# Optimization experiments

Hardware: AMD Instinct MI355X
Metric: run time of the kernel (lower is better)

Reference implementation:

```python
import jax, jax.numpy as jnp
import numpy as np

B, N, M, H, NH = 8, 1024, 512, 1024, 4
DH = H // NH          # 256 main attention head size
CDH = (H // 4) // 4   # 64  cross attention qk head size
EPS = 1e-12


def _ln(x, g, b):
    mu = jnp.mean(x, axis=-1, keepdims=True)
    var = jnp.mean((x - mu) ** 2, axis=-1, keepdims=True)
    return (x - mu) / jnp.sqrt(var + EPS) * g + b


def _heads(x, nh):
    b, n, d = x.shape
    return x.reshape(b, n, nh, d // nh).transpose(0, 2, 1, 3)  # [b,nh,n,dh]


def setup_inputs() -> dict:
    key = jax.random.key(0)
    ks = iter(jax.random.split(key, 64))
    nk = lambda: next(ks)
    w = lambda *s: jax.random.normal(nk(), s, jnp.float32) * 0.02
    inp = {}
    inp["hidden_states"] = jax.random.normal(nk(), (B, N, H), jnp.float32)
    inp["attention_mask"] = jnp.ones((B, N), jnp.float32)
    inp["structure_mask"] = (jax.random.uniform(nk(), (B, 3, N, N)) < 0.2).astype(jnp.float32)
    inp["Sentence_em"] = w(1, B, N, H)
    inp["entity_id_em"] = w(1, B, N, H)
    inp["cross_struct_mask"] = (jax.random.uniform(nk(), (B, 1, N, M)) < 0.3).astype(jnp.float32)
    inp["encoder_hidden_states"] = jax.random.normal(nk(), (1, B, M, H), jnp.float32)
    inp["encoder_attention_mask"] = jnp.ones((B, M), jnp.float32)
    # ---- Struct_SelfAttention params ----
    inp["Wq"] = w(H, 3 * DH); inp["bq"] = jnp.zeros(3 * DH)
    inp["Wk"] = w(H, 3 * DH); inp["bk"] = jnp.zeros(3 * DH)
    inp["Wv"] = w(H, H);      inp["bv"] = jnp.zeros(H)
    inp["Wq1"] = w(H, DH);    inp["bq1"] = jnp.zeros(DH)
    inp["Wk1"] = w(H, DH);    inp["bk1"] = jnp.zeros(DH)
    inp["ln_g"] = jnp.ones(H); inp["ln_b"] = jnp.zeros(H)
    inp["gnn_W"] = w(H, H); inp["gnn_b"] = jnp.zeros(H)
    inp["gnn_ln_g"] = jnp.ones(H); inp["gnn_ln_b"] = jnp.zeros(H)
    # ---- Cross_Attention params ----
    inp["cWq"] = w(H, H // 4); inp["cbq"] = jnp.zeros(H // 4)
    inp["cWk"] = w(H, H // 4); inp["cbk"] = jnp.zeros(H // 4)
    inp["cWv"] = w(H, H);      inp["cbv"] = jnp.zeros(H)
    inp["cWo"] = w(H, H);      inp["cbo"] = jnp.zeros(H)
    inp["cWg"] = w(2 * H, H);  inp["cbg"] = jnp.full((H,), -1.0, jnp.float32)  # Gate bias init -1
    inp["c_ln_g"] = jnp.ones(H); inp["c_ln_b"] = jnp.zeros(H)
    # ---- Output block params ----
    inp["oW1"] = w(H, H); inp["ob1"] = jnp.zeros(H)
    inp["o_ln1_g"] = jnp.ones(H); inp["o_ln1_b"] = jnp.zeros(H)
    inp["oW2"] = w(H, 2 * H); inp["ob2"] = jnp.zeros(2 * H)
    inp["oW3"] = w(2 * H, H); inp["ob3"] = jnp.zeros(H)
    inp["o_ln3_g"] = jnp.ones(H); inp["o_ln3_b"] = jnp.zeros(H)
    inp["layer_idx"] = 0
    return inp


def reference(hidden_states, attention_mask, structure_mask, Sentence_em, entity_id_em,
              cross_struct_mask, encoder_hidden_states, encoder_attention_mask,
              Wq, bq, Wk, bk, Wv, bv, Wq1, bq1, Wk1, bk1, ln_g, ln_b,
              gnn_W, gnn_b, gnn_ln_g, gnn_ln_b,
              cWq, cbq, cWk, cbk, cWv, cbv, cWo, cbo, cWg, cbg, c_ln_g, c_ln_b,
              oW1, ob1, o_ln1_g, o_ln1_b, oW2, ob2, oW3, ob3, o_ln3_g, o_ln3_b,
              layer_idx):
    hs = hidden_states
    q = _heads(hs @ Wq + bq, 3)          # [B,3,N,DH]
    k = _heads(hs @ Wk + bk, 3)
    v = _heads(hs @ Wv + bv, 4)          # [B,4,N,DH]
    s1 = jnp.einsum('bhnd,bhmd->bhnm', q, k)          # unscaled scores, 3 heads
    am0 = (1.0 - attention_mask)[:, None, None, :] * -10000.0
    s3 = s1 + am0
    # valid off-diagonal pairs mask (broadcasts over the 3 heads)
    pair = attention_mask[:, None, :, None] * attention_mask[:, None, None, :]
    idxw = ((pair * (1.0 - jnp.eye(N, dtype=jnp.float32))) > 0.5).astype(jnp.float32)  # [B,1,N,N]
    # sigmoid focal loss (gamma=2, alpha=0.25, mean over selected elements)
    p = jax.nn.sigmoid(s3)
    t = structure_mask
    fl = 0.25 * t * (1.0 - p) ** 2 * (-jax.nn.log_sigmoid(s3)) \
       + 0.75 * (1.0 - t) * p ** 2 * (-jax.nn.log_sigmoid(-s3))
    loss = jnp.sum(fl * idxw) / (3.0 * jnp.sum(idxw))
    # structural attention path (3 heads)
    s1 = s1 / np.float32(np.sqrt(DH)) + (1.0 - structure_mask) * -10000.0
    probs1 = jax.nn.softmax(s1, axis=-1)
    # positional/structural single-head path
    h1 = _ln(hs + Sentence_em[layer_idx] + entity_id_em[layer_idx], ln_g, ln_b)
    q1 = _heads(h1 @ Wq1 + bq1, 1)
    k1 = _heads(h1 @ Wk1 + bk1, 1)
    s2 = jnp.einsum('bhnd,bhmd->bhnm', q1, k1) / np.float32(np.sqrt(DH)) + am0
    probs2 = jax.nn.softmax(s2, axis=-1)
    probs = jnp.concatenate([probs2, probs1], axis=1)  # [B,4,N,N]
    ctx = jnp.einsum('bhnm,bhmd->bhnd', probs, v).transpose(0, 2, 1, 3).reshape(B, N, H)
    gnn_out = _ln(ctx @ gnn_W + gnn_b, gnn_ln_g, gnn_ln_b)
    # ---- Cross attention ----
    enc = encoder_hidden_states[layer_idx]            # [B,M,H]
    cq = _heads(gnn_out @ cWq + cbq, 4)               # [B,4,N,CDH]
    ck = _heads(enc @ cWk + cbk, 4)                   # [B,4,M,CDH]
    cv = _heads(enc @ cWv + cbv, 4)                   # [B,4,M,DH]
    cs = jnp.einsum('bhnd,bhmd->bhnm', cq, ck) / np.float32(np.sqrt(CDH))
    cs = cs + (1.0 - cross_struct_mask) * -10000.0
    cp = jax.nn.softmax(cs, axis=-1)
    cctx = jnp.einsum('bhnm,bhmd->bhnd', cp, cv).transpose(0, 2, 1, 3).reshape(B, N, H)
    cctx = cctx @ cWo + cbo
    gate = jax.nn.sigmoid(jnp.concatenate([gnn_out, cctx], axis=-1) @ cWg + cbg)
    cross_out = _ln(gate * cctx + (1.0 - gate) * gnn_out, c_ln_g, c_ln_b)
    # ---- Output block (gated FFN) ----
    h = _ln(cross_out @ oW1 + ob1 + hidden_states, o_ln1_g, o_ln1_b)
    h3 = jax.nn.gelu(h @ oW2 + ob2, approximate=False) @ oW3 + ob3
    out = _ln(h3 + h, o_ln3_g, o_ln3_b)
    return out, loss
```

## Files before the change

### kernel.cpp

```cpp
#include <hip/hip_runtime.h>
#include <math.h>

#define DEV __device__ __forceinline__

typedef short short8 __attribute__((ext_vector_type(8)));
typedef float float4v __attribute__((ext_vector_type(4)));

DEV unsigned short f2bf(float f) {
    union { float f; unsigned u; } v; v.f = f;
    unsigned r = v.u + 0x7FFFu + ((v.u >> 16) & 1u);
    return (unsigned short)(r >> 16);
}

DEV float block_reduce(float v, int mode) {
    #pragma unroll
    for (int off = 32; off; off >>= 1) {
        float o = __shfl_xor(v, off);
        v = mode ? fmaxf(v, o) : (v + o);
    }
    __shared__ float sbuf[4];
    __syncthreads();
    if ((threadIdx.x & 63) == 0) sbuf[threadIdx.x >> 6] = v;
    __syncthreads();
    float r = sbuf[0];
    #pragma unroll
    for (int w = 1; w < 4; w++) r = mode ? fmaxf(r, sbuf[w]) : (r + sbuf[w]);
    return r;
}

template <bool BIAS, bool ACCUM, bool GELU>
__global__ __launch_bounds__(256) void gemm_bf16_kernel(
    const unsigned short* __restrict__ A, int lda,
    const unsigned short* __restrict__ Bt, int ldb,
    const float* __restrict__ bias,
    float* __restrict__ Cf, unsigned short* __restrict__ Cb,
    int N, int K)
{
    __shared__ unsigned short As[128 * 40];
    __shared__ unsigned short Bs[128 * 40];
    const int tid = threadIdx.x;
    const int w = tid >> 6, lane = tid & 63;
    const int l15 = lane & 15, quad = lane >> 4;
    const int m0 = blockIdx.y * 128, n0 = blockIdx.x * 128;
    const int wm = (w >> 1) * 64, wn = (w & 1) * 64;

    float4v acc[4][4];
    #pragma unroll
    for (int i = 0; i < 4; i++)
        #pragma unroll
        for (int j = 0; j < 4; j++) acc[i][j] = (float4v){0.f, 0.f, 0.f, 0.f};

    for (int k0 = 0; k0 < K; k0 += 32) {
        __syncthreads();
        #pragma unroll
        for (int i = 0; i < 2; i++) {
            const int c = tid + i * 256;
            const int row = c >> 2, kc = (c & 3) * 8;
            *(uint4*)(As + row * 40 + kc) =
                *(const uint4*)(A + (size_t)(m0 + row) * lda + k0 + kc);
            *(uint4*)(Bs + row * 40 + kc) =
                *(const uint4*)(Bt + (size_t)(n0 + row) * ldb + k0 + kc);
        }
        __syncthreads();
        short8 Af[4], Bf[4];
        #pragma unroll
        for (int mt = 0; mt < 4; mt++)
            Af[mt] = *(const short8*)(As + (wm + mt * 16 + l15) * 40 + quad * 8);
        #pragma unroll
        for (int nt = 0; nt < 4; nt++)
            Bf[nt] = *(const short8*)(Bs + (wn + nt * 16 + l15) * 40 + quad * 8);
        #pragma unroll
        for (int mt = 0; mt < 4; mt++)
            #pragma unroll
            for (int nt = 0; nt < 4; nt++)
                acc[mt][nt] = __builtin_amdgcn_mfma_f32_16x16x32_bf16(
                    Af[mt], Bf[nt], acc[mt][nt], 0, 0, 0);
    }

    #pragma unroll
    for (int nt = 0; nt < 4; nt++) {
        const int n = n0 + wn + nt * 16 + l15;
        const float bv = BIAS ? bias[n] : 0.f;
        #pragma unroll
        for (int mt = 0; mt < 4; mt++) {
            #pragma unroll
            for (int r = 0; r < 4; r++) {
                const int m = m0 + wm + mt * 16 + quad * 4 + r;
                const size_t off = (size_t)m * N + n;
                float v = acc[mt][nt][r] + bv;
                if (ACCUM) v += Cf[off];
                if (GELU) v = 0.5f * v * (1.f + erff(v * 0.70710678118654752f));
                if (Cf) Cf[off] = v;
                if (Cb) Cb[off] = f2bf(v);
            }
        }
    }
}

__global__ __launch_bounds__(256) void wtrans_kernel(
    const float* __restrict__ W, unsigned short* __restrict__ Wt, int K, int N)
{
    __shared__ float t[32][33];
    const int n0 = blockIdx.x * 32, k0 = blockIdx.y * 32;
    const int c = threadIdx.x & 31, r8 = threadIdx.x >> 5;
    #pragma unroll
    for (int i = 0; i < 4; i++) {
        const int r = r8 + i * 8;
        t[r][c] = W[(size_t)(k0 + r) * N + n0 + c];
    }
    __syncthreads();
    #pragma unroll
    for (int i = 0; i < 4; i++) {
        const int r = r8 + i * 8;
        Wt[(size_t)(n0 + r) * K + k0 + c] = f2bf(t[c][r]);
    }
}

__global__ __launch_bounds__(256) void trans_kernel(
    const unsigned short* __restrict__ v, unsigned short* __restrict__ Vt,
    int R, int C)
{
    __shared__ unsigned short t[32][33];
    const int b = blockIdx.z, r0 = blockIdx.x * 32, c0 = blockIdx.y * 32;
    const int c = threadIdx.x & 31, r8 = threadIdx.x >> 5;
    #pragma unroll
    for (int i = 0; i < 4; i++) {
        const int r = r8 + i * 8;
        t[r][c] = v[((size_t)b * R + r0 + r) * C + c0 + c];
    }
    __syncthreads();
    #pragma unroll
    for (int i = 0; i < 4; i++) {
        const int r = r8 + i * 8;
        Vt[((size_t)b * C + c0 + r) * R + r0 + c] = t[c][r];
    }
}

__global__ __launch_bounds__(256) void castbf_kernel(
    const float* __restrict__ x, unsigned short* __restrict__ y)
{
    const size_t i = ((size_t)blockIdx.x * 256 + threadIdx.x) * 4;
    float4 v = *(const float4*)(x + i);
    ushort4 o;
    o.x = f2bf(v.x); o.y = f2bf(v.y); o.z = f2bf(v.z); o.w = f2bf(v.w);
    *(ushort4*)(y + i) = o;
}

DEV void ln_finish(float4 xv, const float* __restrict__ g,
                   const float* __restrict__ bb, float* __restrict__ outf,
                   unsigned short* __restrict__ outb, size_t base)
{
    float s  = xv.x + xv.y + xv.z + xv.w;
    float s2 = xv.x * xv.x + xv.y * xv.y + xv.z * xv.z + xv.w * xv.w;
    #pragma unroll
    for (int off = 32; off; off >>= 1) {
        s += __shfl_xor(s, off);
        s2 += __shfl_xor(s2, off);
    }
    __shared__ float sa[4], sb[4];
    if ((threadIdx.x & 63) == 0) {
        sa[threadIdx.x >> 6] = s; sb[threadIdx.x >> 6] = s2;
    }
    __syncthreads();
    s  = sa[0] + sa[1] + sa[2] + sa[3];
    s2 = sb[0] + sb[1] + sb[2] + sb[3];
    const float mu  = s * (1.f / 1024.f);
    const float var = fmaxf(s2 * (1.f / 1024.f) - mu * mu, 0.f);
    const float inv = rsqrtf(var + 1e-12f);
    const int tid = threadIdx.x;
    float4 gv = ((const float4*)g)[tid];
    float4 bv = ((const float4*)bb)[tid];
    float4 o;
    o.x = (xv.x - mu) * inv * gv.x + bv.x;
    o.y = (xv.y - mu) * inv * gv.y + bv.y;
    o.z = (xv.z - mu) * inv * gv.z + bv.z;
    o.w = (xv.w - mu) * inv * gv.w + bv.w;
    if (outf) ((float4*)(outf + base))[tid] = o;
    if (outb) {
        ushort4 ob;
        ob.x = f2bf(o.x); ob.y = f2bf(o.y); ob.z = f2bf(o.z); ob.w = f2bf(o.w);
        ((ushort4*)(outb + base))[tid] = ob;
    }
}

__global__ __launch_bounds__(256) void ln_kernel(
    const float* __restrict__ x, const float* __restrict__ r1,
    const float* __restrict__ r2, const float* __restrict__ g,
    const float* __restrict__ bb, float* __restrict__ outf,
    unsigned short* __restrict__ outb)
{
    const size_t base = (size_t)blockIdx.x * 1024;
    const int tid = threadIdx.x;
    float4 xv = ((const float4*)(x + base))[tid];
    if (r1) {
        float4 a = ((const float4*)(r1 + base))[tid];
        xv.x += a.x; xv.y += a.y; xv.z += a.z; xv.w += a.w;
    }
    if (r2) {
        float4 a = ((const float4*)(r2 + base))[tid];
        xv.x += a.x; xv.y += a.y; xv.z += a.z; xv.w += a.w;
    }
    ln_finish(xv, g, bb, outf, outb, base);
}

__global__ __launch_bounds__(256) void gate_ln_kernel(
    const float* __restrict__ gpre, const float* __restrict__ co,
    const float* __restrict__ gn, const float* __restrict__ g,
    const float* __restrict__ bb, float* __restrict__ outf,
    unsigned short* __restrict__ outb)
{
    const size_t base = (size_t)blockIdx.x * 1024;
    const int tid = threadIdx.x;
    float4 gp = ((const float4*)(gpre + base))[tid];
    float4 cv = ((const float4*)(co + base))[tid];
    float4 gv = ((const float4*)(gn + base))[tid];
    float4 xv; float s;
    s = 1.f / (1.f + __expf(-gp.x)); xv.x = s * cv.x + (1.f - s) * gv.x;
    s = 1.f / (1.f + __expf(-gp.y)); xv.y = s * cv.y + (1.f - s) * gv.y;
    s = 1.f / (1.f + __expf(-gp.z)); xv.z = s * cv.z + (1.f - s) * gv.z;
    s = 1.f / (1.f + __expf(-gp.w)); xv.w = s * cv.w + (1.f - s) * gv.w;
    ln_finish(xv, g, bb, outf, outb, base);
}

__global__ __launch_bounds__(256) void attn_mfma_kernel(
    const unsigned short* __restrict__ qh,
    const unsigned short* __restrict__ kh,
    const unsigned short* __restrict__ q1,
    const unsigned short* __restrict__ k1,
    const unsigned short* __restrict__ Vt,
    const float* __restrict__ am,
    const float* __restrict__ smask,
    unsigned short* __restrict__ ctx,
    float* __restrict__ nump, float* __restrict__ denp)
{
    const int nb = blockIdx.x;
    const int h  = blockIdx.y;
    const int b  = blockIdx.z;
    const int tid = threadIdx.x;
    const int w = tid >> 6, lane = tid & 63;
    const int l15 = lane & 15, quad = lane >> 4;
    const int n0 = nb * 64;

    __shared__ unsigned short Ks[32 * 264];
    __shared__ unsigned short Vs[256 * 40];
    __shared__ unsigned short Ps[4][16 * 40];

    const unsigned short* qsrc; const unsigned short* ksrc; int kpitch, koff;
    if (h == 0) { qsrc = q1; ksrc = k1; kpitch = 256; koff = 0; }
    else        { qsrc = qh; ksrc = kh; kpitch = 768; koff = (h - 1) * 256; }

    short8 Qf[8];
    {
        const unsigned short* qrow =
            qsrc + (size_t)(b * 1024 + n0 + w * 16 + l15) * kpitch + koff;
        #pragma unroll
        for (int kk = 0; kk < 8; kk++)
            Qf[kk] = *(const short8*)(qrow + kk * 32 + quad * 8);
    }

    float4v O[16];
    #pragma unroll
    for (int i = 0; i < 16; i++) O[i] = (float4v){0.f, 0.f, 0.f, 0.f};
    float lsum[4] = {0.f, 0.f, 0.f, 0.f};
    float flsum = 0.f, dencnt = 0.f;
    const int nrow_base = n0 + w * 16 + quad * 4;
    float amn[4];
    #pragma unroll
    for (int r = 0; r < 4; r++) amn[r] = am[b * 1024 + nrow_base + r];
    const float* smbase = (h > 0)
        ? smask + ((size_t)b * 3 + (h - 1)) * 1024 * 1024 : nullptr;

    for (int m0 = 0; m0 < 1024; m0 += 32) {
        __syncthreads();
        for (int c = tid; c < 1024; c += 256) {
            const int row = c >> 5, kc = (c & 31) * 8;
            *(uint4*)(Ks + row * 264 + kc) =
                *(const uint4*)(ksrc + (size_t)(b * 1024 + m0 + row) * kpitch + koff + kc);
        }
        for (int c = tid; c < 1024; c += 256) {
            const int d = c >> 2, mc = (c & 3) * 8;
            *(uint4*)(Vs + d * 40 + mc) =
                *(const uint4*)(Vt + (size_t)(b * 1024 + h * 256 + d) * 1024 + m0 + mc);
        }
        __syncthreads();

        float4v S[2];
        #pragma unroll
        for (int st = 0; st < 2; st++) {
            float4v a = (float4v){0.f, 0.f, 0.f, 0.f};
            #pragma unroll
            for (int kk = 0; kk < 8; kk++) {
                short8 Kf = *(const short8*)(Ks + (st * 16 + l15) * 264 + kk * 32 + quad * 8);
                a = __builtin_amdgcn_mfma_f32_16x16x32_bf16(Qf[kk], Kf, a, 0, 0, 0);
            }
            S[st] = a;
        }

        float e[2][4];
        #pragma unroll
        for (int st = 0; st < 2; st++) {
            const int mcol = m0 + st * 16 + l15;
            const float amm = am[b * 1024 + mcol];
            const float am0 = (1.f - amm) * (-10000.f);
            #pragma unroll
            for (int r = 0; r < 4; r++) {
                const float sraw = S[st][r];
                float scv;
                if (h > 0) {
                    const int nrow = nrow_base + r;
                    const float t  = smbase[(size_t)nrow * 1024 + mcol];
                    const float s3 = sraw + am0;
                    const float idxw =
                        ((amn[r] * amm * ((mcol == nrow) ? 0.f : 1.f)) > 0.5f) ? 1.f : 0.f;
                    const float E = __expf(-fabsf(s3));
                    const float L = __logf(1.f + E);
                    const float R = 1.f / (1.f + E);
                    const float p = (s3 >= 0.f) ? R : E * R;
                    const float sp = fmaxf(s3, 0.f) + L;
                    const float omp = 1.f - p;
                    flsum += idxw * (0.25f * t * omp * omp * (sp - s3)
                                   + 0.75f * (1.f - t) * p * p * sp);
                    dencnt += idxw;
                    scv = sraw * 0.0625f + (1.f - t) * (-10000.f);
                } else {
                    scv = sraw * 0.0625f + am0;
                }
                const float ev = __expf(fminf(scv, 30.f));
                e[st][r] = ev;
                lsum[r] += ev;
            }
        }

        #pragma unroll
        for (int st = 0; st < 2; st++)
            #pragma unroll
            for (int r = 0; r < 4; r++)
                Ps[w][(quad * 4 + r) * 40 + st * 16 + l15] = f2bf(e[st][r]);
        const short8 Pf = *(const short8*)(&Ps[w][l15 * 40 + quad * 8]);
        #pragma unroll
        for (int dt = 0; dt < 16; dt++) {
            short8 Vf = *(const short8*)(Vs + (dt * 16 + l15) * 40 + quad * 8);
            O[dt] = __builtin_amdgcn_mfma_f32_16x16x32_bf16(Pf, Vf, O[dt], 0, 0, 0);
        }
    }

    float rinv[4];
    #pragma unroll
    for (int r = 0; r < 4; r++) {
        float s = lsum[r];
        #pragma unroll
        for (int off = 8; off; off >>= 1) s += __shfl_xor(s, off);
        rinv[r] = 1.f / s;
    }
    #pragma unroll
    for (int dt = 0; dt < 16; dt++)
        #pragma unroll
        for (int r = 0; r < 4; r++)
            ctx[(size_t)(b * 1024 + nrow_base + r) * 1024 + h * 256 + dt * 16 + l15]
                = f2bf(O[dt][r] * rinv[r]);

    if (h > 0) {
        const float fb = block_reduce(flsum, 0);
        if (tid == 0) nump[(b * 3 + (h - 1)) * 16 + nb] = fb;
        if (h == 1) {
            const float db = block_reduce(dencnt, 0);
            if (tid == 0) denp[b * 16 + nb] = db;
        }
    }
}

__global__ __launch_bounds__(256) void cross_mfma_kernel(
    const unsigned short* __restrict__ cq,
    const unsigned short* __restrict__ ck,
    const unsigned short* __restrict__ cvt,
    const float* __restrict__ csm,
    unsigned short* __restrict__ cctx)
{
    const int nb = blockIdx.x;
    const int h  = blockIdx.y;
    const int b  = blockIdx.z;
    const int tid = threadIdx.x;
    const int w = tid >> 6, lane = tid & 63;
    const int l15 = lane & 15, quad = lane >> 4;
    const int n0 = nb * 64;

    __shared__ unsigned short Ks[32 * 72];
    __shared__ unsigned short Vs[256 * 40];
    __shared__ unsigned short Ps[4][16 * 40];

    short8 Qf[2];
    {
        const unsigned short* qrow =
            cq + (size_t)(b * 1024 + n0 + w * 16 + l15) * 256 + h * 64;
        #pragma unroll
        for (int kk = 0; kk < 2; kk++)
            Qf[kk] = *(const short8*)(qrow + kk * 32 + quad * 8);
    }

    float4v O[16];
    #pragma unroll
    for (int i = 0; i < 16; i++) O[i] = (float4v){0.f, 0.f, 0.f, 0.f};
    float lsum[4] = {0.f, 0.f, 0.f, 0.f};
    const int nrow_base = n0 + w * 16 + quad * 4;

    for (int m0 = 0; m0 < 512; m0 += 32) {
        __syncthreads();
        if (tid < 256) {
            const int row = tid >> 3, kc = (tid & 7) * 8;
            *(uint4*)(Ks + row * 72 + kc) =
                *(const uint4*)(ck + (size_t)(b * 512 + m0 + row) * 256 + h * 64 + kc);
        }
        for (int c = tid; c < 1024; c += 256) {
            const int d = c >> 2, mc = (c & 3) * 8;
            *(uint4*)(Vs + d * 40 + mc) =
                *(const uint4*)(cvt + (size_t)(b * 1024 + h * 256 + d) * 512 + m0 + mc);
        }
        __syncthreads();

        float e[2][4];
        #pragma unroll
        for (int st = 0; st < 2; st++) {
            float4v a = (float4v){0.f, 0.f, 0.f, 0.f};
            #pragma unroll
            for (int kk = 0; kk < 2; kk++) {
                short8 Kf = *(const short8*)(Ks + (st * 16 + l15) * 72 + kk * 32 + quad * 8);
                a = __builtin_amdgcn_mfma_f32_16x16x32_bf16(Qf[kk], Kf, a, 0, 0, 0);
            }
            const int mcol = m0 + st * 16 + l15;
            #pragma unroll
            for (int r = 0; r < 4; r++) {
                const float msk = csm[(size_t)(b * 1024 + nrow_base + r) * 512 + mcol];
                const float scv = a[r] * 0.125f + (1.f - msk) * (-10000.f);
                const float ev = __expf(fminf(scv, 30.f));
                e[st][r] = ev;
                lsum[r] += ev;
            }
        }

        #pragma unroll
        for (int st = 0; st < 2; st++)
            #pragma unroll
            for (int r = 0; r < 4; r++)
                Ps[w][(quad * 4 + r) * 40 + st * 16 + l15] = f2bf(e[st][r]);
        const short8 Pf = *(const short8*)(&Ps[w][l15 * 40 + quad * 8]);
        #pragma unroll
        for (int dt = 0; dt < 16; dt++) {
            short8 Vf = *(const short8*)(Vs + (dt * 16 + l15) * 40 + quad * 8);
            O[dt] = __builtin_amdgcn_mfma_f32_16x16x32_bf16(Pf, Vf, O[dt], 0, 0, 0);
        }
    }

    float rinv[4];
    #pragma unroll
    for (int r = 0; r < 4; r++) {
        float s = lsum[r];
        #pragma unroll
        for (int off = 8; off; off >>= 1) s += __shfl_xor(s, off);
        rinv[r] = 1.f / s;
    }
    #pragma unroll
    for (int dt = 0; dt < 16; dt++)
        #pragma unroll
        for (int r = 0; r < 4; r++)
            cctx[(size_t)(b * 1024 + nrow_base + r) * 1024 + h * 256 + dt * 16 + l15]
                = f2bf(O[dt][r] * rinv[r]);
}

__global__ __launch_bounds__(256) void loss_reduce_kernel(
    const float* __restrict__ nump, const float* __restrict__ denp,
    float* __restrict__ out)
{
    __shared__ double sn[256], sd[256];
    const int tid = threadIdx.x;
    double ns = 0.0, ds = 0.0;
    for (int i = tid; i < 384; i += 256) ns += (double)nump[i];
    for (int i = tid; i < 128; i += 256) ds += (double)denp[i];
    sn[tid] = ns; sd[tid] = ds;
    __syncthreads();
    for (int off = 128; off; off >>= 1) {
        if (tid < off) { sn[tid] += sn[tid + off]; sd[tid] += sd[tid + off]; }
        __syncthreads();
    }
    if (tid == 0) out[0] = (float)(sn[0] / (3.0 * sd[0]));
}

extern "C" void kernel_launch(void* const* d_in, const int* in_sizes, int n_in,
                              void* d_out, int out_size, void* d_ws, size_t ws_size,
                              hipStream_t stream)
{
    (void)in_sizes; (void)n_in; (void)out_size; (void)ws_size;
    const float* hs   = (const float*)d_in[0];
    const float* am   = (const float*)d_in[1];
    const float* smask= (const float*)d_in[2];
    const float* sent = (const float*)d_in[3];
    const float* ent  = (const float*)d_in[4];
    const float* csm  = (const float*)d_in[5];
    const float* enc  = (const float*)d_in[6];
    const float* Wq  = (const float*)d_in[8];  const float* bq  = (const float*)d_in[9];
    const float* Wk  = (const float*)d_in[10]; const float* bk  = (const float*)d_in[11];
    const float* Wv  = (const float*)d_in[12]; const float* bv  = (const float*)d_in[13];
    const float* Wq1 = (const float*)d_in[14]; const float* bq1 = (const float*)d_in[15];
    const float* Wk1 = (const float*)d_in[16]; const float* bk1 = (const float*)d_in[17];
    const float* ln_g= (const float*)d_in[18]; const float* ln_b= (const float*)d_in[19];
    const float* gW  = (const float*)d_in[20]; const float* gb  = (const float*)d_in[21];
    const float* gng = (const float*)d_in[22]; const float* gnb = (const float*)d_in[23];
    const float* cWq = (const float*)d_in[24]; const float* cbq = (const float*)d_in[25];
    const float* cWk = (const float*)d_in[26]; const float* cbk = (const float*)d_in[27];
    const float* cWv = (const float*)d_in[28]; const float* cbv = (const float*)d_in[29];
    const float* cWo = (const float*)d_in[30]; const float* cbo = (const float*)d_in[31];
    const float* cWg = (const float*)d_in[32]; const float* cbg = (const float*)d_in[33];
    const float* clg = (const float*)d_in[34]; const float* clb = (const float*)d_in[35];
    const float* oW1 = (const float*)d_in[36]; const float* ob1 = (const float*)d_in[37];
    const float* l1g = (const float*)d_in[38]; const float* l1b = (const float*)d_in[39];
    const float* oW2 = (const float*)d_in[40]; const float* ob2 = (const float*)d_in[41];
    const float* oW3 = (const float*)d_in[42]; const float* ob3 = (const float*)d_in[43];
    const float* l3g = (const float*)d_in[44]; const float* l3b = (const float*)d_in[45];
    float* out = (float*)d_out;

    typedef unsigned short ush;
    char* wsb = (char*)d_ws;
    ush* WT   = (ush*)wsb;
    ush* wqT  = WT;             ush* wkT  = WT + 786432;   ush* wvT  = WT + 1572864;
    ush* wq1T = WT + 2621440;   ush* wk1T = WT + 2883584;  ush* gWT_ = WT + 3145728;
    ush* cWqT = WT + 4194304;   ush* cWkT = WT + 4456448;  ush* cWvT = WT + 4718592;
    ush* cWoT = WT + 5767168;   ush* cWgT = WT + 6815744;  ush* oW1T = WT + 8912896;
    ush* oW2T = WT + 9961472;   ush* oW3T = WT + 12058624;
    ush*  hs_bf   = (ush*)(wsb + 28311552);
    ush*  enc_bf  = (ush*)(wsb + 45088768);
    ush*  q_bf    = (ush*)(wsb + 53477376);
    ush*  k_bf    = (ush*)(wsb + 66060288);
    ush*  v_bf    = (ush*)(wsb + 78643200);
    ush*  Vt      = (ush*)(wsb + 95420416);
    ush*  h1_bf   = (ush*)(wsb + 112197632);
    ush*  q1_bf   = (ush*)(wsb + 128974848);
    ush*  k1_bf   = (ush*)(wsb + 133169152);
    ush*  ctx_bf  = (ush*)(wsb + 137363456);
    float* nump   = (float*)(wsb + 154140672);
    float* denp   = (float*)(wsb + 154142208);
    float* gnn_f  = (float*)(wsb + 154144768);
    float* gnnout_f = (float*)(wsb + 187699200);
    ush*  gnnout_b  = (ush*)(wsb + 221253632);
    ush*  cq_b      = (ush*)(wsb + 53477376);
    ush*  ck_b      = (ush*)(wsb + 66060288);
    ush*  cv_b      = (ush*)(wsb + 78643200);
    ush*  cctx_b    = (ush*)(wsb + 95420416);
    ush*  cvt       = (ush*)(wsb + 238030848);
    float* cctxo_f  = (float*)(wsb + 154144768);
    ush*  cctxo_b   = (ush*)(wsb + 28311552);
    float* gatepre_f= (float*)(wsb + 112197632);
    ush*  crossout_b= (ush*)(wsb + 221253632);
    float* t_f      = (float*)(wsb + 154144768);
    float* h_f      = (float*)(wsb + 187699200);
    ush*  h_b       = (ush*)(wsb + 28311552);
    ush*  h2g_b     = (ush*)(wsb + 45088768);
    float* h3_f     = (float*)(wsb + 154144768);

    dim3 blk(256);
    castbf_kernel<<<8192, blk, 0, stream>>>(hs, hs_bf);
    castbf_kernel<<<4096, blk, 0, stream>>>(enc, enc_bf);
    wtrans_kernel<<<dim3(768/32, 1024/32), blk, 0, stream>>>(Wq, wqT, 1024, 768);
    wtrans_kernel<<<dim3(768/32, 1024/32), blk, 0, stream>>>(Wk, wkT, 1024, 768);
    wtrans_kernel<<<dim3(32, 32), blk, 0, stream>>>(Wv, wvT, 1024, 1024);
    wtrans_kernel<<<dim3(8, 32), blk, 0, stream>>>(Wq1, wq1T, 1024, 256);
    wtrans_kernel<<<dim3(8, 32), blk, 0, stream>>>(Wk1, wk1T, 1024, 256);
    wtrans_kernel<<<dim3(32, 32), blk, 0, stream>>>(gW, gWT_, 1024, 1024);
    wtrans_kernel<<<dim3(8, 32), blk, 0, stream>>>(cWq, cWqT, 1024, 256);
    wtrans_kernel<<<dim3(8, 32), blk, 0, stream>>>(cWk, cWkT, 1024, 256);
    wtrans_kernel<<<dim3(32, 32), blk, 0, stream>>>(cWv, cWvT, 1024, 1024);
    wtrans_kernel<<<dim3(32, 32), blk, 0, stream>>>(cWo, cWoT, 1024, 1024);
    wtrans_kernel<<<dim3(32, 64), blk, 0, stream>>>(cWg, cWgT, 2048, 1024);
    wtrans_kernel<<<dim3(32, 32), blk, 0, stream>>>(oW1, oW1T, 1024, 1024);
    wtrans_kernel<<<dim3(64, 32), blk, 0, stream>>>(oW2, oW2T, 1024, 2048);
    wtrans_kernel<<<dim3(32, 64), blk, 0, stream>>>(oW3, oW3T, 2048, 1024);
    gemm_bf16_kernel<true,false,false><<<dim3(6, 64), blk, 0, stream>>>(
        hs_bf, 1024, wqT, 1024, bq, nullptr, q_bf, 768, 1024);
    gemm_bf16_kernel<true,false,false><<<dim3(6, 64), blk, 0, stream>>>(
        hs_bf, 1024, wkT, 1024, bk, nullptr, k_bf, 768, 1024);
    gemm_bf16_kernel<true,false,false><<<dim3(8, 64), blk, 0, stream>>>(
        hs_bf, 1024, wvT, 1024, bv, nullptr, v_bf, 1024, 1024);
    ln_kernel<<<8192, blk, 0, stream>>>(hs, sent, ent, ln_g, ln_b, nullptr, h1_bf);
    gemm_bf16_kernel<true,false,false><<<dim3(2, 64), blk, 0, stream>>>(
        h1_bf, 1024, wq1T, 1024, bq1, nullptr, q1_bf, 256, 1024);
    gemm_bf16_kernel<true,false,false><<<dim3(2, 64), blk, 0, stream>>>(
        h1_bf, 1024, wk1T, 1024, bk1, nullptr, k1_bf, 256, 1024);
    trans_kernel<<<dim3(32, 32, 8), blk, 0, stream>>>(v_bf, Vt, 1024, 1024);
    attn_mfma_kernel<<<dim3(16, 4, 8), blk, 0, stream>>>(
        q_bf, k_bf, q1_bf, k1_bf, Vt, am, smask, ctx_bf, nump, denp);
    loss_reduce_kernel<<<1, blk, 0, stream>>>(nump, denp, out + 8388608);
    gemm_bf16_kernel<true,false,false><<<dim3(8, 64), blk, 0, stream>>>(
        ctx_bf, 1024, gWT_, 1024, gb, gnn_f, nullptr, 1024, 1024);
    ln_kernel<<<8192, blk, 0, stream>>>(gnn_f, nullptr, nullptr, gng, gnb,
                                        gnnout_f, gnnout_b);
    gemm_bf16_kernel<true,false,false><<<dim3(2, 64), blk, 0, stream>>>(
        gnnout_b, 1024, cWqT, 1024, cbq, nullptr, cq_b, 256, 1024);
    gemm_bf16_kernel<true,false,false><<<dim3(2, 32), blk, 0, stream>>>(
        enc_bf, 1024, cWkT, 1024, cbk, nullptr, ck_b, 256, 1024);
    gemm_bf16_kernel<true,false,false><<<dim3(8, 32), blk, 0, stream>>>(
        enc_bf, 1024, cWvT, 1024, cbv, nullptr, cv_b, 1024, 1024);
    trans_kernel<<<dim3(16, 32, 8), blk, 0, stream>>>(cv_b, cvt, 512, 1024);
    cross_mfma_kernel<<<dim3(16, 4, 8), blk, 0, stream>>>(
        cq_b, ck_b, cvt, csm, cctx_b);
    gemm_bf16_kernel<true,false,false><<<dim3(8, 64), blk, 0, stream>>>(
        cctx_b, 1024, cWoT, 1024, cbo, cctxo_f, cctxo_b, 1024, 1024);
    gemm_bf16_kernel<true,false,false><<<dim3(8, 64), blk, 0, stream>>>(
        gnnout_b, 1024, cWgT, 2048, cbg, gatepre_f, nullptr, 1024, 1024);
    gemm_bf16_kernel<false,true,false><<<dim3(8, 64), blk, 0, stream>>>(
        cctxo_b, 1024, cWgT + 1024, 2048, nullptr, gatepre_f, nullptr, 1024, 1024);
    gate_ln_kernel<<<8192, blk, 0, stream>>>(gatepre_f, cctxo_f, gnnout_f,
                                             clg, clb, nullptr, crossout_b);
    gemm_bf16_kernel<true,false,false><<<dim3(8, 64), blk, 0, stream>>>(
        crossout_b, 1024, oW1T, 1024, ob1, t_f, nullptr, 1024, 1024);
    ln_kernel<<<8192, blk, 0, stream>>>(t_f, hs, nullptr, l1g, l1b, h_f, h_b);
    gemm_bf16_kernel<true,false,true><<<dim3(16, 64), blk, 0, stream>>>(
        h_b, 1024, oW2T, 1024, ob2, nullptr, h2g_b, 2048, 1024);
    gemm_bf16_kernel<true,false,false><<<dim3(8, 64), blk, 0, stream>>>(
        h2g_b, 2048, oW3T, 2048, ob3, h3_f, nullptr, 1024, 2048);
    ln_kernel<<<8192, blk, 0, stream>>>(h3_f, h_f, nullptr, l3g, l3b, out, nullptr);
}
```

Before: 1.314 ms.

## Prefetch K/V tiles in registers, batch weight transposes, fuse gate GEMM via concat

The attention and cross-attention kernels now load the next K/V tile into registers while computing the current one, hiding global-load latency behind the MFMA work. The fourteen weight-transpose launches are merged into one table-driven kernel to cut launch overhead. The gnn_out and cctx bf16 outputs are written into a shared concatenated buffer with a 2048 pitch, so the gate projection runs as a single K=2048 GEMM instead of two GEMMs with a read-modify-write accumulation. The register prefetch adds register pressure, which may lower occupancy in the attention kernels.

Result: slower. 1.469 ms (+11.8%).

```diff
diff --git a/kernel.cpp b/kernel.cpp
--- a/kernel.cpp
+++ b/kernel.cpp
@@ -33,7 +33,7 @@
     const unsigned short* __restrict__ A, int lda,
     const unsigned short* __restrict__ Bt, int ldb,
     const float* __restrict__ bias,
-    float* __restrict__ Cf, unsigned short* __restrict__ Cb,
+    float* __restrict__ Cf, unsigned short* __restrict__ Cb, int cbp,
     int N, int K)
 {
     __shared__ unsigned short As[128 * 40];
@@ -91,28 +91,40 @@
                 if (ACCUM) v += Cf[off];
                 if (GELU) v = 0.5f * v * (1.f + erff(v * 0.70710678118654752f));
                 if (Cf) Cf[off] = v;
-                if (Cb) Cb[off] = f2bf(v);
+                if (Cb) Cb[(size_t)m * cbp + n] = f2bf(v);
             }
         }
     }
 }
 
-__global__ __launch_bounds__(256) void wtrans_kernel(
-    const float* __restrict__ W, unsigned short* __restrict__ Wt, int K, int N)
-{
-    __shared__ float t[32][33];
-    const int n0 = blockIdx.x * 32, k0 = blockIdx.y * 32;
+struct WtDesc { const float* W; unsigned short* Wt; int K; int N; int base; };
+struct WtTable { WtDesc d[14]; };
+
+__global__ __launch_bounds__(256) void wtrans_all_kernel(WtTable tab)
+{
+    const int bid = blockIdx.x;
+    int s = 0;
+    #pragma unroll
+    for (int i = 1; i < 14; i++) if (bid >= tab.d[i].base) s = i;
+    const float* W = tab.d[s].W;
+    unsigned short* Wt = tab.d[s].Wt;
+    const int K = tab.d[s].K, N = tab.d[s].N;
+    const int t = bid - tab.d[s].base;
+    const int ntn = N >> 5;
+    const int n0 = (t % ntn) * 32, k0 = (t / ntn) * 32;
+
+    __shared__ float tbuf[32][33];
     const int c = threadIdx.x & 31, r8 = threadIdx.x >> 5;
     #pragma unroll
     for (int i = 0; i < 4; i++) {
         const int r = r8 + i * 8;
-        t[r][c] = W[(size_t)(k0 + r) * N + n0 + c];
+        tbuf[r][c] = W[(size_t)(k0 + r) * N + n0 + c];
     }
     __syncthreads();
     #pragma unroll
     for (int i = 0; i < 4; i++) {
         const int r = r8 + i * 8;
-        Wt[(size_t)(n0 + r) * K + k0 + c] = f2bf(t[c][r]);
+        Wt[(size_t)(n0 + r) * K + k0 + c] = f2bf(tbuf[c][r]);
     }
 }
 
@@ -148,7 +160,7 @@
 
 DEV void ln_finish(float4 xv, const float* __restrict__ g,
                    const float* __restrict__ bb, float* __restrict__ outf,
-                   unsigned short* __restrict__ outb, size_t base)
+                   unsigned short* __restrict__ outb, size_t basef, size_t baseb)
 {
     float s  = xv.x + xv.y + xv.z + xv.w;
     float s2 = xv.x * xv.x + xv.y * xv.y + xv.z * xv.z + xv.w * xv.w;
@@ -175,11 +187,11 @@
     o.y = (xv.y - mu) * inv * gv.y + bv.y;
     o.z = (xv.z - mu) * inv * gv.z + bv.z;
     o.w = (xv.w - mu) * inv * gv.w + bv.w;
-    if (outf) ((float4*)(outf + base))[tid] = o;
+    if (outf) ((float4*)(outf + basef))[tid] = o;
     if (outb) {
         ushort4 ob;
         ob.x = f2bf(o.x); ob.y = f2bf(o.y); ob.z = f2bf(o.z); ob.w = f2bf(o.w);
-        ((ushort4*)(outb + base))[tid] = ob;
+        ((ushort4*)(outb + baseb))[tid] = ob;
     }
 }
 
@@ -187,7 +199,7 @@
     const float* __restrict__ x, const float* __restrict__ r1,
     const float* __restrict__ r2, const float* __restrict__ g,
     const float* __restrict__ bb, float* __restrict__ outf,
-    unsigned short* __restrict__ outb)
+    unsigned short* __restrict__ outb, int obp)
 {
     const size_t base = (size_t)blockIdx.x * 1024;
     const int tid = threadIdx.x;
@@ -200,7 +212,7 @@
         float4 a = ((const float4*)(r2 + base))[tid];
         xv.x += a.x; xv.y += a.y; xv.z += a.z; xv.w += a.w;
     }
-    ln_finish(xv, g, bb, outf, outb, base);
+    ln_finish(xv, g, bb, outf, outb, base, (size_t)blockIdx.x * obp);
 }
 
 __global__ __launch_bounds__(256) void gate_ln_kernel(
@@ -219,7 +231,7 @@
     s = 1.f / (1.f + __expf(-gp.y)); xv.y = s * cv.y + (1.f - s) * gv.y;
     s = 1.f / (1.f + __expf(-gp.z)); xv.z = s * cv.z + (1.f - s) * gv.z;
     s = 1.f / (1.f + __expf(-gp.w)); xv.w = s * cv.w + (1.f - s) * gv.w;
-    ln_finish(xv, g, bb, outf, outb, base);
+    ln_finish(xv, g, bb, outf, outb, base, base);
 }
 
 __global__ __launch_bounds__(256) void attn_mfma_kernel(
@@ -258,6 +270,16 @@
             Qf[kk] = *(const short8*)(qrow + kk * 32 + quad * 8);
     }
 
+    uint4 kreg[4], vreg[4];
+    #pragma unroll
+    for (int i = 0; i < 4; i++) {
+        const int c = tid + i * 256;
+        kreg[i] = *(const uint4*)(ksrc + (size_t)(b * 1024 + (c >> 5)) * kpitch
+                                  + koff + (c & 31) * 8);
+        vreg[i] = *(const uint4*)(Vt + (size_t)(b * 1024 + h * 256 + (c >> 2)) * 1024
+                                  + (c & 3) * 8);
+    }
+
     float4v O[16];
     #pragma unroll
     for (int i = 0; i < 16; i++) O[i] = (float4v){0.f, 0.f, 0.f, 0.f};
@@ -270,19 +292,27 @@
     const float* smbase = (h > 0)
         ? smask + ((size_t)b * 3 + (h - 1)) * 1024 * 1024 : nullptr;
 
-    for (int m0 = 0; m0 < 1024; m0 += 32) {
+    for (int step = 0; step < 32; step++) {
+        const int m0 = step * 32;
         __syncthreads();
-        for (int c = tid; c < 1024; c += 256) {
-            const int row = c >> 5, kc = (c & 31) * 8;
-            *(uint4*)(Ks + row * 264 + kc) =
-                *(const uint4*)(ksrc + (size_t)(b * 1024 + m0 + row) * kpitch + koff + kc);
-        }
-        for (int c = tid; c < 1024; c += 256) {
-            const int d = c >> 2, mc = (c & 3) * 8;
-            *(uint4*)(Vs + d * 40 + mc) =
-                *(const uint4*)(Vt + (size_t)(b * 1024 + h * 256 + d) * 1024 + m0 + mc);
+        #pragma unroll
+        for (int i = 0; i < 4; i++) {
+            const int c = tid + i * 256;
+            *(uint4*)(Ks + (c >> 5) * 264 + (c & 31) * 8) = kreg[i];
+            *(uint4*)(Vs + (c >> 2) * 40 + (c & 3) * 8) = vreg[i];
         }
         __syncthreads();
+        if (step < 31) {
+            const int m1 = m0 + 32;
+            #pragma unroll
+            for (int i = 0; i < 4; i++) {
+                const int c = tid + i * 256;
+                kreg[i] = *(const uint4*)(ksrc + (size_t)(b * 1024 + m1 + (c >> 5)) * kpitch
+                                          + koff + (c & 31) * 8);
+                vreg[i] = *(const uint4*)(Vt + (size_t)(b * 1024 + h * 256 + (c >> 2)) * 1024
+                                          + m1 + (c & 3) * 8);
+            }
+        }
 
         float4v S[2];
         #pragma unroll
@@ -397,25 +427,43 @@
             Qf[kk] = *(const short8*)(qrow + kk * 32 + quad * 8);
     }
 
+    uint4 kreg, vreg[4];
+    kreg = *(const uint4*)(ck + (size_t)(b * 512 + (tid >> 3)) * 256 + h * 64
+                           + (tid & 7) * 8);
+    #pragma unroll
+    for (int i = 0; i < 4; i++) {
+        const int c = tid + i * 256;
+        vreg[i] = *(const uint4*)(cvt + (size_t)(b * 1024 + h * 256 + (c >> 2)) * 512
+                                  + (c & 3) * 8);
+    }
+
     float4v O[16];
     #pragma unroll
     for (int i = 0; i < 16; i++) O[i] = (float4v){0.f, 0.f, 0.f, 0.f};
     float lsum[4] = {0.f, 0.f, 0.f, 0.f};
     const int nrow_base = n0 + w * 16 + quad * 4;
 
-    for (int m0 = 0; m0 < 512; m0 += 32) {
+    for (int step = 0; step < 16; step++) {
+        const int m0 = step * 32;
         __syncthreads();
-        if (tid < 256) {
-            const int row = tid >> 3, kc = (tid & 7) * 8;
-            *(uint4*)(Ks + row * 72 + kc) =
-                *(const uint4*)(ck + (size_t)(b * 512 + m0 + row) * 256 + h * 64 + kc);
-        }
-        for (int c = tid; c < 1024; c += 256) {
-            const int d = c >> 2, mc = (c & 3) * 8;
-            *(uint4*)(Vs + d * 40 + mc) =
-                *(const uint4*)(cvt + (size_t)(b * 1024 + h * 256 + d) * 512 + m0 + mc);
+        *(uint4*)(Ks + (tid >> 3) * 72 + (tid & 7) * 8) = kreg;
+        #pragma unroll
+        for (int i = 0; i < 4; i++) {
+            const int c = tid + i * 256;
+            *(uint4*)(Vs + (c >> 2) * 40 + (c & 3) * 8) = vreg[i];
         }
         __syncthreads();
+        if (step < 15) {
+            const int m1 = m0 + 32;
+            kreg = *(const uint4*)(ck + (size_t)(b * 512 + m1 + (tid >> 3)) * 256
+                                   + h * 64 + (tid & 7) * 8);
+            #pragma unroll
+            for (int i = 0; i < 4; i++) {
+                const int c = tid + i * 256;
+                vreg[i] = *(const uint4*)(cvt + (size_t)(b * 1024 + h * 256 + (c >> 2)) * 512
+                                          + m1 + (c & 3) * 8);
+            }
+        }
 
         float e[2][4];
         #pragma unroll
@@ -539,14 +587,13 @@
     float* denp   = (float*)(wsb + 154142208);
     float* gnn_f  = (float*)(wsb + 154144768);
     float* gnnout_f = (float*)(wsb + 187699200);
-    ush*  gnnout_b  = (ush*)(wsb + 221253632);
+    ush*  concat_b  = (ush*)(wsb + 221253632);
+    ush*  cvt       = (ush*)(wsb + 254808064);
     ush*  cq_b      = (ush*)(wsb + 53477376);
     ush*  ck_b      = (ush*)(wsb + 66060288);
     ush*  cv_b      = (ush*)(wsb + 78643200);
     ush*  cctx_b    = (ush*)(wsb + 95420416);
-    ush*  cvt       = (ush*)(wsb + 238030848);
     float* cctxo_f  = (float*)(wsb + 154144768);
-    ush*  cctxo_b   = (ush*)(wsb + 28311552);
     float* gatepre_f= (float*)(wsb + 112197632);
     ush*  crossout_b= (ush*)(wsb + 221253632);
     float* t_f      = (float*)(wsb + 154144768);
@@ -558,62 +605,62 @@
     dim3 blk(256);
     castbf_kernel<<<8192, blk, 0, stream>>>(hs, hs_bf);
     castbf_kernel<<<4096, blk, 0, stream>>>(enc, enc_bf);
-    wtrans_kernel<<<dim3(768/32, 1024/32), blk, 0, stream>>>(Wq, wqT, 1024, 768);
-    wtrans_kernel<<<dim3(768/32, 1024/32), blk, 0, stream>>>(Wk, wkT, 1024, 768);
-    wtrans_kernel<<<dim3(32, 32), blk, 0, stream>>>(Wv, wvT, 1024, 1024);
-    wtrans_kernel<<<dim3(8, 32), blk, 0, stream>>>(Wq1, wq1T, 1024, 256);
-    wtrans_kernel<<<dim3(8, 32), blk, 0, stream>>>(Wk1, wk1T, 1024, 256);
-    wtrans_kernel<<<dim3(32, 32), blk, 0, stream>>>(gW, gWT_, 1024, 1024);
-    wtrans_kernel<<<dim3(8, 32), blk, 0, stream>>>(cWq, cWqT, 1024, 256);
-    wtrans_kernel<<<dim3(8, 32), blk, 0, stream>>>(cWk, cWkT, 1024, 256);
-    wtrans_kernel<<<dim3(32, 32), blk, 0, stream>>>(cWv, cWvT, 1024, 1024);
-    wtrans_kernel<<<dim3(32, 32), blk, 0, stream>>>(cWo, cWoT, 1024, 1024);
-    wtrans_kernel<<<dim3(32, 64), blk, 0, stream>>>(cWg, cWgT, 2048, 1024);
-    wtrans_kernel<<<dim3(32, 32), blk, 0, stream>>>(oW1, oW1T, 1024, 1024);
-    wtrans_kernel<<<dim3(64, 32), blk, 0, stream>>>(oW2, oW2T, 1024, 2048);
-    wtrans_kernel<<<dim3(32, 64), blk, 0, stream>>>(oW3, oW3T, 2048, 1024);
+    {
+        WtTable tab; int idx = 0, base = 0;
+        auto addw = [&](const float* W, ush* Wt, int K, int N) {
+            tab.d[idx].W = W; tab.d[idx].Wt = Wt; tab.d[idx].K = K;
+            tab.d[idx].N = N; tab.d[idx].base = base;
+            base += (K / 32) * (N / 32); idx++;
+        };
+        addw(Wq,  wqT,  1024, 768);  addw(Wk,  wkT,  1024, 768);
+        addw(Wv,  wvT,  1024, 1024); addw(Wq1, wq1T, 1024, 256);
+        addw(Wk1, wk1T, 1024, 256);  addw(gW,  gWT_, 1024, 1024);
+        addw(cWq, cWqT, 1024, 256);  addw(cWk, cWkT, 1024, 256);
+        addw(cWv, cWvT, 1024, 1024); addw(cWo, cWoT, 1024, 1024);
+        addw(cWg, cWgT, 2048, 1024); addw(oW1, oW1T, 1024, 1024);
+        addw(oW2, oW2T, 1024, 2048); addw(oW3, oW3T, 2048, 1024);
+        wtrans_all_kernel<<<base, blk, 0, stream>>>(tab);
+    }
     gemm_bf16_kernel<true,false,false><<<dim3(6, 64), blk, 0, stream>>>(
-        hs_bf, 1024, wqT, 1024, bq, nullptr, q_bf, 768, 1024);
+        hs_bf, 1024, wqT, 1024, bq, nullptr, q_bf, 768, 768, 1024);
     gemm_bf16_kernel<true,false,false><<<dim3(6, 64), blk, 0, stream>>>(
-        hs_bf, 1024, wkT, 1024, bk, nullptr, k_bf, 768, 1024);
+        hs_bf, 1024, wkT, 1024, bk, nullptr, k_bf, 768, 768, 1024);
     gemm_bf16_kernel<true,false,false><<<dim3(8, 64), blk, 0, stream>>>(
-        hs_bf, 1024, wvT, 1024, bv, nullptr, v_bf, 1024, 1024);
-    ln_kernel<<<8192, blk, 0, stream>>>(hs, sent, ent, ln_g, ln_b, nullptr, h1_bf);
+        hs_bf, 1024, wvT, 1024, bv, nullptr, v_bf, 1024, 1024, 1024);
+    ln_kernel<<<8192, blk, 0, stream>>>(hs, sent, ent, ln_g, ln_b, nullptr, h1_bf, 1024);
     gemm_bf16_kernel<true,false,false><<<dim3(2, 64), blk, 0, stream>>>(
-        h1_bf, 1024, wq1T, 1024, bq1, nullptr, q1_bf, 256, 1024);
+        h1_bf, 1024, wq1T, 1024, bq1, nullptr, q1_bf, 256, 256, 1024);
     gemm_bf16_kernel<true,false,false><<<dim3(2, 64), blk, 0, stream>>>(
-        h1_bf, 1024, wk1T, 1024, bk1, nullptr, k1_bf, 256, 1024);
+        h1_bf, 1024, wk1T, 1024, bk1, nullptr, k1_bf, 256, 256, 1024);
     trans_kernel<<<dim3(32, 32, 8), blk, 0, stream>>>(v_bf, Vt, 1024, 1024);
     attn_mfma_kernel<<<dim3(16, 4, 8), blk, 0, stream>>>(
         q_bf, k_bf, q1_bf, k1_bf, Vt, am, smask, ctx_bf, nump, denp);
     loss_reduce_kernel<<<1, blk, 0, stream>>>(nump, denp, out + 8388608);
     gemm_bf16_kernel<true,false,false><<<dim3(8, 64), blk, 0, stream>>>(
-        ctx_bf, 1024, gWT_, 1024, gb, gnn_f, nullptr, 1024, 1024);
+        ctx_bf, 1024, gWT_, 1024, gb, gnn_f, nullptr, 1024, 1024, 1024);
     ln_kernel<<<8192, blk, 0, stream>>>(gnn_f, nullptr, nullptr, gng, gnb,
-                                        gnnout_f, gnnout_b);
+                                        gnnout_f, concat_b, 2048);
     gemm_bf16_kernel<true,false,false><<<dim3(2, 64), blk, 0, stream>>>(
-        gnnout_b, 1024, cWqT, 1024, cbq, nullptr, cq_b, 256, 1024);
+        concat_b, 2048, cWqT, 1024, cbq, nullptr, cq_b, 256, 256, 1024);
     gemm_bf16_kernel<true,false,false><<<dim3(2, 32), blk, 0, stream>>>(
-        enc_bf, 1024, cWkT, 1024, cbk, nullptr, ck_b, 256, 1024);
+        enc_bf, 1024, cWkT, 1024, cbk, nullptr, ck_b, 256, 256, 1024);
     gemm_bf16_kernel<true,false,false><<<dim3(8, 32), blk, 0, stream>>>(
-        enc_bf, 1024, cWvT, 1024, cbv, nullptr, cv_b, 1024, 1024);
+        enc_bf, 1024, cWvT, 1024, cbv, nullptr, cv_b, 1024, 1024, 1024);
     trans_kernel<<<dim3(16, 32, 8), blk, 0, stream>>>(cv_b, cvt, 512, 1024);
     cross_mfma_kernel<<<dim3(16, 4, 8), blk, 0, stream>>>(
         cq_b, ck_b, cvt, csm, cctx_b);
     gemm_bf16_kernel<true,false,false><<<dim3(8, 64), blk, 0, stream>>>(
-        cctx_b, 1024, cWoT, 1024, cbo, cctxo_f, cctxo_b, 1024, 1024);
+        cctx_b, 1024, cWoT, 1024, cbo, cctxo_f, concat_b + 1024, 2048, 1024, 1024);
     gemm_bf16_kernel<true,false,false><<<dim3(8, 64), blk, 0, stream>>>(
-        gnnout_b, 1024, cWgT, 2048, cbg, gatepre_f, nullptr, 1024, 1024);
-    gemm_bf16_kernel<false,true,false><<<dim3(8, 64), blk, 0, stream>>>(
-        cctxo_b, 1024, cWgT + 1024, 2048, nullptr, gatepre_f, nullptr, 1024, 1024);
+        concat_b, 2048, cWgT, 2048, cbg, gatepre_f, nullptr, 1024, 1024, 2048);
     gate_ln_kernel<<<8192, blk, 0, stream>>>(gatepre_f, cctxo_f, gnnout_f,
                                              clg, clb, nullptr, crossout_b);
     gemm_bf16_kernel<true,false,false><<<dim3(8, 64), blk, 0, stream>>>(
-        crossout_b, 1024, oW1T, 1024, ob1, t_f, nullptr, 1024, 1024);
-    ln_kernel<<<8192, blk, 0, stream>>>(t_f, hs, nullptr, l1g, l1b, h_f, h_b);
+        crossout_b, 1024, oW1T, 1024, ob1, t_f, nullptr, 1024, 1024, 1024);
+    ln_kernel<<<8192, blk, 0, stream>>>(t_f, hs, nullptr, l1g, l1b, h_f, h_b, 1024);
     gemm_bf16_kernel<true,false,true><<<dim3(16, 64), blk, 0, stream>>>(
-        h_b, 1024, oW2T, 1024, ob2, nullptr, h2g_b, 2048, 1024);
+        h_b, 1024, oW2T, 1024, ob2, nullptr, h2g_b, 2048, 2048, 1024);
     gemm_bf16_kernel<true,false,false><<<dim3(8, 64), blk, 0, stream>>>(
-        h2g_b, 2048, oW3T, 2048, ob3, h3_f, nullptr, 1024, 2048);
-    ln_kernel<<<8192, blk, 0, stream>>>(h3_f, h_f, nullptr, l3g, l3b, out, nullptr);
-}
+        h2g_b, 2048, oW3T, 2048, ob3, h3_f, nullptr, 1024, 1024, 2048);
+    ln_kernel<<<8192, blk, 0, stream>>>(h3_f, h_f, nullptr, l3g, l3b, out, nullptr, 1024);
+}
```
